# Kernel optimization log

Measured on AMD Instinct MI355X. Metric: run time of the kernel, lower is better.

## Reference

```python
import jax, jax.numpy as jnp
import numpy as np

ALPHA = 1.0

def setup_inputs() -> dict:
    key = jax.random.key(0)
    k1, k2 = jax.random.split(key)
    N, K, D = 131072, 100, 256
    z = jax.random.normal(k1, (N, D), dtype=jnp.float32)
    # xavier_normal_ for a (K, D) parameter: std = sqrt(2/(K+D))
    std = np.sqrt(2.0 / (K + D)).astype(np.float32)
    cluster_layer = jax.random.normal(k2, (K, D), dtype=jnp.float32) * std
    return {"z": z, "cluster_layer": cluster_layer}

def reference(z, cluster_layer):
    # squared distances via ||z||^2 + ||c||^2 - 2 z.c  (avoids [N,K,D] intermediate)
    z2 = jnp.sum(z * z, axis=1, keepdims=True)              # [N,1]
    c2 = jnp.sum(cluster_layer * cluster_layer, axis=1)     # [K]
    d2 = z2 + c2[None, :] - 2.0 * (z @ cluster_layer.T)     # [N,K]
    d2 = jnp.maximum(d2, 0.0)
    q = 1.0 / (1.0 + d2 / ALPHA)
    q = q ** ((ALPHA + 1.0) / 2.0)                          # no-op for alpha=1, kept for fidelity
    q = q / jnp.sum(q, axis=1, keepdims=True)               # row normalize
    return q
```

## Files before the change

kernel.cpp:

```cpp
#include <hip/hip_runtime.h>


typedef __attribute__((ext_vector_type(8))) _Float16 f16x8;
typedef __attribute__((ext_vector_type(4))) float    f32x4;

#define DDIM 256
#define KCL  100
#define KPAD 112
#define NT   7

__global__ __launch_bounds__(512, 4) void cluster_q(const float* __restrict__ z,
                                                    const float* __restrict__ cl,
                                                    float* __restrict__ out) {
    __shared__ _Float16 Bs[KPAD * DDIM];
    __shared__ float    c2s[KPAD];

    const int tid  = threadIdx.x;
    const int lane = tid & 63;
    const int wv   = tid >> 6;
    const int g    = lane >> 4;
    const int c16  = lane & 15;

    const long rowbase = (long)blockIdx.x * 256 + wv * 32;

    const float* p0 = z + (rowbase + c16) * DDIM + 4 * g;
    const float* p1 = p0 + 16 * DDIM;

    f32x4 lo0 = *reinterpret_cast<const f32x4*>(p0);
    f32x4 hi0 = *reinterpret_cast<const f32x4*>(p0 + 16);
    f32x4 lo1 = *reinterpret_cast<const f32x4*>(p1);
    f32x4 hi1 = *reinterpret_cast<const f32x4*>(p1 + 16);

    #pragma unroll
    for (int j = 0; j < 7; ++j) {
        const int idx = j * 512 + tid;
        const int r   = idx >> 5;
        const int cw  = idx & 31;
        const int offA = 32 * (cw >> 2) + 4 * (cw & 3);
        f32x4 a = {0.f, 0.f, 0.f, 0.f}, b = {0.f, 0.f, 0.f, 0.f};
        if (r < KCL) {
            const float* base = cl + r * DDIM;
            a = *reinterpret_cast<const f32x4*>(base + offA);
            b = *reinterpret_cast<const f32x4*>(base + offA + 16);
        }
        f16x8 v;
        v[0] = (_Float16)a[0]; v[1] = (_Float16)a[1];
        v[2] = (_Float16)a[2]; v[3] = (_Float16)a[3];
        v[4] = (_Float16)b[0]; v[5] = (_Float16)b[1];
        v[6] = (_Float16)b[2]; v[7] = (_Float16)b[3];
        *reinterpret_cast<f16x8*>(reinterpret_cast<char*>(Bs)
            + r * 512 + ((cw * 16) ^ ((r & 7) << 4))) = v;

        float ss = a[0]*a[0] + a[1]*a[1] + a[2]*a[2] + a[3]*a[3]
                 + b[0]*b[0] + b[1]*b[1] + b[2]*b[2] + b[3]*b[3];
        ss += __shfl_xor(ss, 1);
        ss += __shfl_xor(ss, 2);
        ss += __shfl_xor(ss, 4);
        ss += __shfl_xor(ss, 8);
        ss += __shfl_xor(ss, 16);
        if ((lane & 31) == 0) c2s[r] = ss;
    }
    __syncthreads();

    f32x4 acc[2][NT];
    #pragma unroll
    for (int i = 0; i < 2; ++i)
        #pragma unroll
        for (int t = 0; t < NT; ++t)
            acc[i][t] = f32x4{0.f, 0.f, 0.f, 0.f};

    float zsq[2] = {0.f, 0.f};

    const int rx = (c16 & 7) << 4;
    const char* bbase = reinterpret_cast<const char*>(Bs) + c16 * 512;

    #pragma unroll 1
    for (int s = 0; s < 8; ++s) {
        const int kn = (s < 7) ? 32 * (s + 1) : 0;
        f32x4 nlo0 = *reinterpret_cast<const f32x4*>(p0 + kn);
        f32x4 nhi0 = *reinterpret_cast<const f32x4*>(p0 + kn + 16);
        f32x4 nlo1 = *reinterpret_cast<const f32x4*>(p1 + kn);
        f32x4 nhi1 = *reinterpret_cast<const f32x4*>(p1 + kn + 16);

        zsq[0] += lo0[0]*lo0[0] + lo0[1]*lo0[1] + lo0[2]*lo0[2] + lo0[3]*lo0[3]
                + hi0[0]*hi0[0] + hi0[1]*hi0[1] + hi0[2]*hi0[2] + hi0[3]*hi0[3];
        zsq[1] += lo1[0]*lo1[0] + lo1[1]*lo1[1] + lo1[2]*lo1[2] + lo1[3]*lo1[3]
                + hi1[0]*hi1[0] + hi1[1]*hi1[1] + hi1[2]*hi1[2] + hi1[3]*hi1[3];

        f16x8 a0, a1;
        a0[0] = (_Float16)lo0[0]; a0[1] = (_Float16)lo0[1];
        a0[2] = (_Float16)lo0[2]; a0[3] = (_Float16)lo0[3];
        a0[4] = (_Float16)hi0[0]; a0[5] = (_Float16)hi0[1];
        a0[6] = (_Float16)hi0[2]; a0[7] = (_Float16)hi0[3];
        a1[0] = (_Float16)lo1[0]; a1[1] = (_Float16)lo1[1];
        a1[2] = (_Float16)lo1[2]; a1[3] = (_Float16)lo1[3];
        a1[4] = (_Float16)hi1[0]; a1[5] = (_Float16)hi1[1];
        a1[6] = (_Float16)hi1[2]; a1[7] = (_Float16)hi1[3];

        const int sb = (64 * s + 16 * g) ^ rx;
        #pragma unroll
        for (int t = 0; t < NT; ++t) {
            f16x8 b = *reinterpret_cast<const f16x8*>(bbase + t * 16 * 512 + sb);
            acc[0][t] = __builtin_amdgcn_mfma_f32_16x16x32_f16(a0, b, acc[0][t], 0, 0, 0);
            acc[1][t] = __builtin_amdgcn_mfma_f32_16x16x32_f16(a1, b, acc[1][t], 0, 0, 0);
        }

        lo0 = nlo0; hi0 = nhi0; lo1 = nlo1; hi1 = nhi1;
    }

    #pragma unroll
    for (int i = 0; i < 2; ++i) {
        zsq[i] += __shfl_xor(zsq[i], 16);
        zsq[i] += __shfl_xor(zsq[i], 32);
    }

    float c2v[NT];
    #pragma unroll
    for (int t = 0; t < NT; ++t) c2v[t] = c2s[t * 16 + c16];

    __syncthreads();

    float* sc = reinterpret_cast<float*>(reinterpret_cast<char*>(Bs) + wv * 6400);

    #pragma unroll
    for (int i = 0; i < 2; ++i) {
        #pragma unroll
        for (int j = 0; j < 4; ++j) {
            const int r = 4 * g + j;
            const float z2 = __shfl(zsq[i], r);
            float qv[NT];
            float rs = 0.f;
            #pragma unroll
            for (int t = 0; t < NT; ++t) {
                const float dot = acc[i][t][j];
                const float d2 = fmaxf(z2 + c2v[t] - 2.f * dot, 0.f);
                const float q = __builtin_amdgcn_rcpf(1.f + d2);
                qv[t] = q;
                if (t < 6 || c16 < 4) rs += q;
            }
            rs += __shfl_xor(rs, 1);
            rs += __shfl_xor(rs, 2);
            rs += __shfl_xor(rs, 4);
            rs += __shfl_xor(rs, 8);
            const float rinv = __builtin_amdgcn_rcpf(rs);

            #pragma unroll
            for (int t = 0; t < NT; ++t) {
                const int col = t * 16 + c16;
                if (col < KCL) sc[r * KCL + col] = qv[t] * rinv;
            }
        }
        const long gbase = (rowbase + i * 16) * (long)KCL;
        #pragma unroll
        for (int c = 0; c < 7; ++c) {
            const int off = c * 256 + lane * 4;
            if (off < 1600) {
                f32x4 v = *reinterpret_cast<const f32x4*>(sc + off);
                *reinterpret_cast<f32x4*>(out + gbase + off) = v;
            }
        }
    }
}

extern "C" void kernel_launch(void* const* d_in, const int* in_sizes, int n_in,
                              void* d_out, int out_size, void* d_ws, size_t ws_size,
                              hipStream_t stream) {
    const float* z  = (const float*)d_in[0];
    const float* cl = (const float*)d_in[1];
    float* out = (float*)d_out;

    const int N = in_sizes[0] / DDIM;

    cluster_q<<<N / 256, 512, 0, stream>>>(z, cl, out);
}
```

Baseline: 37.98 us.

## Use 1024-thread blocks and process row panels sequentially with dedicated scratch

Doubles the block to 16 waves covering 512 rows, so the centroid fp16 conversion into shared memory is amortized over twice as many rows. Each wave now handles its two 16-row panels one after the other with a single accumulator set, which cuts register pressure but serializes work that was previously interleaved. The epilogue uses a separate 100KB shared scratch buffer, dropping the second barrier. Shared memory rises to about 160KB per block, which likely limits residency to one block per CU.

```diff
diff --git a/kernel.cpp b/kernel.cpp
--- a/kernel.cpp
+++ b/kernel.cpp
@@ -9,10 +9,11 @@
 #define KPAD 112
 #define NT   7
 
-__global__ __launch_bounds__(512, 4) void cluster_q(const float* __restrict__ z,
-                                                    const float* __restrict__ cl,
-                                                    float* __restrict__ out) {
+__global__ __launch_bounds__(1024, 4) void cluster_q(const float* __restrict__ z,
+                                                     const float* __restrict__ cl,
+                                                     float* __restrict__ out) {
     __shared__ _Float16 Bs[KPAD * DDIM];
+    __shared__ float    scr[16 * 1600];
     __shared__ float    c2s[KPAD];
 
     const int tid  = threadIdx.x;
@@ -21,118 +22,124 @@
     const int g    = lane >> 4;
     const int c16  = lane & 15;
 
-    const long rowbase = (long)blockIdx.x * 256 + wv * 32;
+    const long rowbase = (long)blockIdx.x * 512 + wv * 32;
 
-    const float* p0 = z + (rowbase + c16) * DDIM + 4 * g;
-    const float* p1 = p0 + 16 * DDIM;
+    const float* pA = z + (rowbase + c16) * DDIM + 4 * g;
 
-    f32x4 lo0 = *reinterpret_cast<const f32x4*>(p0);
-    f32x4 hi0 = *reinterpret_cast<const f32x4*>(p0 + 16);
-    f32x4 lo1 = *reinterpret_cast<const f32x4*>(p1);
-    f32x4 hi1 = *reinterpret_cast<const f32x4*>(p1 + 16);
+    f32x4 c0lo = *reinterpret_cast<const f32x4*>(pA);
+    f32x4 c0hi = *reinterpret_cast<const f32x4*>(pA + 16);
+    f32x4 c1lo = *reinterpret_cast<const f32x4*>(pA + 32);
+    f32x4 c1hi = *reinterpret_cast<const f32x4*>(pA + 48);
 
     #pragma unroll
-    for (int j = 0; j < 7; ++j) {
-        const int idx = j * 512 + tid;
-        const int r   = idx >> 5;
-        const int cw  = idx & 31;
-        const int offA = 32 * (cw >> 2) + 4 * (cw & 3);
-        f32x4 a = {0.f, 0.f, 0.f, 0.f}, b = {0.f, 0.f, 0.f, 0.f};
-        if (r < KCL) {
-            const float* base = cl + r * DDIM;
-            a = *reinterpret_cast<const f32x4*>(base + offA);
-            b = *reinterpret_cast<const f32x4*>(base + offA + 16);
+    for (int j = 0; j < 4; ++j) {
+        const int idx = j * 1024 + tid;
+        if (idx < KPAD * 32) {
+            const int r   = idx >> 5;
+            const int cw  = idx & 31;
+            const int offA = 32 * (cw >> 2) + 4 * (cw & 3);
+            f32x4 a = {0.f, 0.f, 0.f, 0.f}, b = {0.f, 0.f, 0.f, 0.f};
+            if (r < KCL) {
+                const float* base = cl + r * DDIM;
+                a = *reinterpret_cast<const f32x4*>(base + offA);
+                b = *reinterpret_cast<const f32x4*>(base + offA + 16);
+            }
+            f16x8 v;
+            v[0] = (_Float16)a[0]; v[1] = (_Float16)a[1];
+            v[2] = (_Float16)a[2]; v[3] = (_Float16)a[3];
+            v[4] = (_Float16)b[0]; v[5] = (_Float16)b[1];
+            v[6] = (_Float16)b[2]; v[7] = (_Float16)b[3];
+            *reinterpret_cast<f16x8*>(reinterpret_cast<char*>(Bs)
+                + r * 512 + ((cw * 16) ^ ((r & 7) << 4))) = v;
+
+            float ss = a[0]*a[0] + a[1]*a[1] + a[2]*a[2] + a[3]*a[3]
+                     + b[0]*b[0] + b[1]*b[1] + b[2]*b[2] + b[3]*b[3];
+            ss += __shfl_xor(ss, 1);
+            ss += __shfl_xor(ss, 2);
+            ss += __shfl_xor(ss, 4);
+            ss += __shfl_xor(ss, 8);
+            ss += __shfl_xor(ss, 16);
+            if ((lane & 31) == 0) c2s[r] = ss;
         }
-        f16x8 v;
-        v[0] = (_Float16)a[0]; v[1] = (_Float16)a[1];
-        v[2] = (_Float16)a[2]; v[3] = (_Float16)a[3];
-        v[4] = (_Float16)b[0]; v[5] = (_Float16)b[1];
-        v[6] = (_Float16)b[2]; v[7] = (_Float16)b[3];
-        *reinterpret_cast<f16x8*>(reinterpret_cast<char*>(Bs)
-            + r * 512 + ((cw * 16) ^ ((r & 7) << 4))) = v;
-
-        float ss = a[0]*a[0] + a[1]*a[1] + a[2]*a[2] + a[3]*a[3]
-                 + b[0]*b[0] + b[1]*b[1] + b[2]*b[2] + b[3]*b[3];
-        ss += __shfl_xor(ss, 1);
-        ss += __shfl_xor(ss, 2);
-        ss += __shfl_xor(ss, 4);
-        ss += __shfl_xor(ss, 8);
-        ss += __shfl_xor(ss, 16);
-        if ((lane & 31) == 0) c2s[r] = ss;
     }
     __syncthreads();
 
-    f32x4 acc[2][NT];
-    #pragma unroll
-    for (int i = 0; i < 2; ++i)
-        #pragma unroll
-        for (int t = 0; t < NT; ++t)
-            acc[i][t] = f32x4{0.f, 0.f, 0.f, 0.f};
-
-    float zsq[2] = {0.f, 0.f};
-
     const int rx = (c16 & 7) << 4;
     const char* bbase = reinterpret_cast<const char*>(Bs) + c16 * 512;
-
-    #pragma unroll 1
-    for (int s = 0; s < 8; ++s) {
-        const int kn = (s < 7) ? 32 * (s + 1) : 0;
-        f32x4 nlo0 = *reinterpret_cast<const f32x4*>(p0 + kn);
-        f32x4 nhi0 = *reinterpret_cast<const f32x4*>(p0 + kn + 16);
-        f32x4 nlo1 = *reinterpret_cast<const f32x4*>(p1 + kn);
-        f32x4 nhi1 = *reinterpret_cast<const f32x4*>(p1 + kn + 16);
-
-        zsq[0] += lo0[0]*lo0[0] + lo0[1]*lo0[1] + lo0[2]*lo0[2] + lo0[3]*lo0[3]
-                + hi0[0]*hi0[0] + hi0[1]*hi0[1] + hi0[2]*hi0[2] + hi0[3]*hi0[3];
-        zsq[1] += lo1[0]*lo1[0] + lo1[1]*lo1[1] + lo1[2]*lo1[2] + lo1[3]*lo1[3]
-                + hi1[0]*hi1[0] + hi1[1]*hi1[1] + hi1[2]*hi1[2] + hi1[3]*hi1[3];
-
-        f16x8 a0, a1;
-        a0[0] = (_Float16)lo0[0]; a0[1] = (_Float16)lo0[1];
-        a0[2] = (_Float16)lo0[2]; a0[3] = (_Float16)lo0[3];
-        a0[4] = (_Float16)hi0[0]; a0[5] = (_Float16)hi0[1];
-        a0[6] = (_Float16)hi0[2]; a0[7] = (_Float16)hi0[3];
-        a1[0] = (_Float16)lo1[0]; a1[1] = (_Float16)lo1[1];
-        a1[2] = (_Float16)lo1[2]; a1[3] = (_Float16)lo1[3];
-        a1[4] = (_Float16)hi1[0]; a1[5] = (_Float16)hi1[1];
-        a1[6] = (_Float16)hi1[2]; a1[7] = (_Float16)hi1[3];
-
-        const int sb = (64 * s + 16 * g) ^ rx;
-        #pragma unroll
-        for (int t = 0; t < NT; ++t) {
-            f16x8 b = *reinterpret_cast<const f16x8*>(bbase + t * 16 * 512 + sb);
-            acc[0][t] = __builtin_amdgcn_mfma_f32_16x16x32_f16(a0, b, acc[0][t], 0, 0, 0);
-            acc[1][t] = __builtin_amdgcn_mfma_f32_16x16x32_f16(a1, b, acc[1][t], 0, 0, 0);
-        }
-
-        lo0 = nlo0; hi0 = nhi0; lo1 = nlo1; hi1 = nhi1;
-    }
-
-    #pragma unroll
-    for (int i = 0; i < 2; ++i) {
-        zsq[i] += __shfl_xor(zsq[i], 16);
-        zsq[i] += __shfl_xor(zsq[i], 32);
-    }
+    float* sc = scr + wv * 1600;
 
     float c2v[NT];
     #pragma unroll
     for (int t = 0; t < NT; ++t) c2v[t] = c2s[t * 16 + c16];
 
-    __syncthreads();
+    #pragma unroll 1
+    for (int P = 0; P < 2; ++P) {
+        const float* pP = pA + P * 16 * DDIM;
 
-    float* sc = reinterpret_cast<float*>(reinterpret_cast<char*>(Bs) + wv * 6400);
+        f32x4 acc[NT];
+        #pragma unroll
+        for (int t = 0; t < NT; ++t) acc[t] = f32x4{0.f, 0.f, 0.f, 0.f};
+        float zsq = 0.f;
 
-    #pragma unroll
-    for (int i = 0; i < 2; ++i) {
+        #pragma unroll 1
+        for (int u = 0; u < 4; ++u) {
+            const int kn = (u < 3) ? 32 * (2 * u + 2) : 0;
+            f32x4 n0lo = *reinterpret_cast<const f32x4*>(pP + kn);
+            f32x4 n0hi = *reinterpret_cast<const f32x4*>(pP + kn + 16);
+            f32x4 n1lo = *reinterpret_cast<const f32x4*>(pP + kn + 32);
+            f32x4 n1hi = *reinterpret_cast<const f32x4*>(pP + kn + 48);
+
+            zsq += c0lo[0]*c0lo[0] + c0lo[1]*c0lo[1] + c0lo[2]*c0lo[2] + c0lo[3]*c0lo[3]
+                 + c0hi[0]*c0hi[0] + c0hi[1]*c0hi[1] + c0hi[2]*c0hi[2] + c0hi[3]*c0hi[3]
+                 + c1lo[0]*c1lo[0] + c1lo[1]*c1lo[1] + c1lo[2]*c1lo[2] + c1lo[3]*c1lo[3]
+                 + c1hi[0]*c1hi[0] + c1hi[1]*c1hi[1] + c1hi[2]*c1hi[2] + c1hi[3]*c1hi[3];
+
+            f16x8 a0, a1;
+            a0[0] = (_Float16)c0lo[0]; a0[1] = (_Float16)c0lo[1];
+            a0[2] = (_Float16)c0lo[2]; a0[3] = (_Float16)c0lo[3];
+            a0[4] = (_Float16)c0hi[0]; a0[5] = (_Float16)c0hi[1];
+            a0[6] = (_Float16)c0hi[2]; a0[7] = (_Float16)c0hi[3];
+            a1[0] = (_Float16)c1lo[0]; a1[1] = (_Float16)c1lo[1];
+            a1[2] = (_Float16)c1lo[2]; a1[3] = (_Float16)c1lo[3];
+            a1[4] = (_Float16)c1hi[0]; a1[5] = (_Float16)c1hi[1];
+            a1[6] = (_Float16)c1hi[2]; a1[7] = (_Float16)c1hi[3];
+
+            const int sb0 = (64 * (2 * u)     + 16 * g) ^ rx;
+            const int sb1 = (64 * (2 * u + 1) + 16 * g) ^ rx;
+            #pragma unroll
+            for (int t = 0; t < NT; ++t) {
+                f16x8 b = *reinterpret_cast<const f16x8*>(bbase + t * 16 * 512 + sb0);
+                acc[t] = __builtin_amdgcn_mfma_f32_16x16x32_f16(a0, b, acc[t], 0, 0, 0);
+            }
+            #pragma unroll
+            for (int t = 0; t < NT; ++t) {
+                f16x8 b = *reinterpret_cast<const f16x8*>(bbase + t * 16 * 512 + sb1);
+                acc[t] = __builtin_amdgcn_mfma_f32_16x16x32_f16(a1, b, acc[t], 0, 0, 0);
+            }
+
+            c0lo = n0lo; c0hi = n0hi; c1lo = n1lo; c1hi = n1hi;
+        }
+
+        if (P == 0) {
+            const float* pN = pA + 16 * DDIM;
+            c0lo = *reinterpret_cast<const f32x4*>(pN);
+            c0hi = *reinterpret_cast<const f32x4*>(pN + 16);
+            c1lo = *reinterpret_cast<const f32x4*>(pN + 32);
+            c1hi = *reinterpret_cast<const f32x4*>(pN + 48);
+        }
+
+        zsq += __shfl_xor(zsq, 16);
+        zsq += __shfl_xor(zsq, 32);
+
         #pragma unroll
         for (int j = 0; j < 4; ++j) {
             const int r = 4 * g + j;
-            const float z2 = __shfl(zsq[i], r);
+            const float z2 = __shfl(zsq, r);
             float qv[NT];
             float rs = 0.f;
             #pragma unroll
             for (int t = 0; t < NT; ++t) {
-                const float dot = acc[i][t][j];
+                const float dot = acc[t][j];
                 const float d2 = fmaxf(z2 + c2v[t] - 2.f * dot, 0.f);
                 const float q = __builtin_amdgcn_rcpf(1.f + d2);
                 qv[t] = q;
@@ -150,7 +157,7 @@
                 if (col < KCL) sc[r * KCL + col] = qv[t] * rinv;
             }
         }
-        const long gbase = (rowbase + i * 16) * (long)KCL;
+        const long gbase = (rowbase + P * 16) * (long)KCL;
         #pragma unroll
         for (int c = 0; c < 7; ++c) {
             const int off = c * 256 + lane * 4;
@@ -171,5 +178,5 @@
 
     const int N = in_sizes[0] / DDIM;
 
-    cluster_q<<<N / 256, 512, 0, stream>>>(z, cl, out);
+    cluster_q<<<N / 512, 1024, 0, stream>>>(z, cl, out);
 }
```

Result: slower. 40.40 us (+6.4%).
